# Optimization experiments

Measured on AMD Instinct MI355X. Metric: run time of the kernel, lower is better.

The kernel has to match this reference:

```python
import jax, jax.numpy as jnp
import numpy as np

EPS = 1e-6
NEG_SLOPE = 0.2


def _basis(J):
    # J: [B,N,E,3] -> R: [B,N,E,3(k: U,V,J rows),3(xyz comp)]
    nJ = J / (jnp.linalg.norm(J, axis=-1, keepdims=True) + EPS)
    sub = nJ[..., :2]
    u_z = -(sub[..., 0] ** 2 + sub[..., 1] ** 2) / (nJ[..., 2] + EPS)
    U = jnp.concatenate([sub, u_z[..., None]], axis=-1)
    U = U / (jnp.linalg.norm(U, axis=-1, keepdims=True) + EPS)
    V = jnp.cross(U, nJ)
    return jnp.stack([U, V, nJ], axis=-2)


def _complex_linear(X, J, A, Bw, Cw):
    R = _basis(J)                                   # [B,N,E,3,3], R[...,k,i]
    RtX = jnp.einsum('bneki,bnek->bnei', R, X)      # (R^T X)_i = sum_k R[k,i] X_k
    # rrtx(i, s) has component k equal to R[...,k,i] * s
    a_term = R[..., 0] * RtX[..., 0:1] + R[..., 1] * RtX[..., 1:2]
    b_term = R[..., 1] * RtX[..., 0:1] - R[..., 0] * RtX[..., 1:2]
    c_term = R[..., 2] * RtX[..., 2:3]
    Y = (jnp.einsum('fe,bnei->bnfi', A, a_term)
         + jnp.einsum('fe,bnei->bnfi', Bw, b_term)
         + jnp.einsum('fe,bnei->bnfi', Cw, c_term))
    return Y                                        # [B,N,F,3]


def _vn_leaky_relu(x, W, negative_slope):
    # x: [B,F,3,N]; W: [F,F] torch Linear weight (out,in)
    d = jnp.einsum('gf,bfin->bgin', W, x)
    dot = jnp.sum(x * d, axis=2, keepdims=True)
    d_norm_sq = jnp.sum(d * d, axis=2, keepdims=True)
    neg_branch = x - (dot / (d_norm_sq + EPS)) * d
    lin = jnp.where(dot >= 0, x, neg_branch)
    return negative_slope * x + (1.0 - negative_slope) * lin


def setup_inputs() -> dict:
    key = jax.random.key(0)
    kX, kJ, kA, kB, kC, kW = jax.random.split(key, 6)
    B, N, E, F = 16, 1024, 256, 256
    X = jax.random.normal(kX, (B, N, E, 3), dtype=jnp.float32)
    J = jax.random.normal(kJ, (B, N, E, 3), dtype=jnp.float32)
    A = jax.random.normal(kA, (F, E), dtype=jnp.float32)
    Bw = jax.random.normal(kB, (F, E), dtype=jnp.float32)
    Cw = jax.random.normal(kC, (F, E), dtype=jnp.float32)
    W = jax.random.normal(kW, (F, F), dtype=jnp.float32) * (1.0 / np.sqrt(F))
    return {"X": X, "J": J, "A": A, "Bw": Bw, "Cw": Cw, "W": W, "device": 0}


def reference(X, J, A, Bw, Cw, W, device):
    Y = _complex_linear(X, J, A, Bw, Cw)            # [B,N,F,3]
    x = jnp.transpose(Y, (0, 2, 3, 1))              # [B,F,3,N]
    return _vn_leaky_relu(x, W, NEG_SLOPE)
```

## Files before the change

kernel.cpp:

```cpp
#include <hip/hip_runtime.h>

typedef __attribute__((ext_vector_type(8))) _Float16 half8;
typedef __attribute__((ext_vector_type(4))) _Float16 half4v;
typedef __attribute__((ext_vector_type(4))) float f32x4;
typedef float f32x4u __attribute__((ext_vector_type(4), aligned(4)));
typedef float f32x2u __attribute__((ext_vector_type(2), aligned(4)));

#define EPSF 1e-6f

__device__ __forceinline__ void glds16(const void* g, void* l) {
    __builtin_amdgcn_global_load_lds(
        (const __attribute__((address_space(1))) unsigned*)g,
        (__attribute__((address_space(3))) unsigned*)l, 16, 0, 0);
}
__device__ __forceinline__ unsigned short h2u(_Float16 h) {
    union { _Float16 h; unsigned short u; } c; c.h = h; return c.u;
}

__global__ __launch_bounds__(256) void prep_kernel(
    const float* __restrict__ A, const float* __restrict__ Bw,
    const float* __restrict__ Cw, const float* __restrict__ W,
    _Float16* __restrict__ Mh, _Float16* __restrict__ Wh)
{
    int f = blockIdx.x, e = threadIdx.x;
    Mh[f * 768 + e]       = (_Float16)A[f * 256 + e];
    Mh[f * 768 + 256 + e] = (_Float16)Bw[f * 256 + e];
    Mh[f * 768 + 512 + e] = (_Float16)Cw[f * 256 + e];
    Wh[f * 256 + e]       = (_Float16)W[f * 256 + e];
}

__global__ __launch_bounds__(512, 4) void fused1_kernel(
    const float* __restrict__ X, const float* __restrict__ Jp,
    const _Float16* __restrict__ Mh, _Float16* __restrict__ Y)
{
    __shared__ char lds[55808];
    const int T_OFF = 32768;
    int tid = threadIdx.x;
    int b  = blockIdx.x >> 5;
    int n0 = (blockIdx.x & 31) * 32;

    auto stageA = [&](int buf, int kt) {
        int eb = kt / 3, t = kt % 3;
        int k0 = t * 256 + eb * 32;
        #pragma unroll
        for (int h = 0; h < 2; ++h) {
            int u = h * 512 + tid;
            int row = u >> 2, slot = u & 3;
            size_t go = ((size_t)row * 768 + k0) * 2 + ((slot * 16) ^ ((row & 3) << 4));
            glds16((const char*)Mh + go, lds + buf * 16384 + u * 16);
        }
    };

    int l = tid & 63, lr = l & 15, lq = l >> 4;
    int w = tid >> 6, wc = w & 1, wf = w >> 1;
    int nl = tid >> 4, ep = tid & 15;

    f32x4 acc[3][4] = {};
    stageA(0, 0);

    for (int eb = 0; eb < 8; ++eb) {
        __syncthreads();
        {
            size_t pbase = ((size_t)((b * 1024 + n0 + nl) * 256) + eb * 32 + 2 * ep) * 3;
            f32x4u xa = *(const f32x4u*)(X + pbase);
            f32x2u xb = *(const f32x2u*)(X + pbase + 4);
            f32x4u ja = *(const f32x4u*)(Jp + pbase);
            f32x2u jb = *(const f32x2u*)(Jp + pbase + 4);
            float xs[6] = { xa[0], xa[1], xa[2], xa[3], xb[0], xb[1] };
            float js[6] = { ja[0], ja[1], ja[2], ja[3], jb[0], jb[1] };
            unsigned short hv[2][9];
            #pragma unroll
            for (int p = 0; p < 2; ++p) {
                float x0 = xs[3*p], x1 = xs[3*p+1], x2 = xs[3*p+2];
                float j0 = js[3*p], j1 = js[3*p+1], j2 = js[3*p+2];
                float jj  = j0*j0 + j1*j1 + j2*j2;
                float rn  = __builtin_amdgcn_rcpf(__builtin_amdgcn_sqrtf(jj) + EPSF);
                float nj0 = j0*rn, nj1 = j1*rn, nj2 = j2*rn;
                float s2  = nj0*nj0 + nj1*nj1;
                float uz  = -s2 * __builtin_amdgcn_rcpf(nj2 + EPSF);
                float ru  = __builtin_amdgcn_rcpf(__builtin_amdgcn_sqrtf(s2 + uz*uz) + EPSF);
                float u0 = nj0*ru, u1 = nj1*ru, u2 = uz*ru;
                float v0 = u1*nj2 - u2*nj1;
                float v1 = u2*nj0 - u0*nj2;
                float v2 = u0*nj1 - u1*nj0;
                float r0 = u0*x0 + v0*x1 + nj0*x2;
                float r1 = u1*x0 + v1*x1 + nj1*x2;
                float r2 = u2*x0 + v2*x1 + nj2*x2;
                hv[p][0] = h2u((_Float16)(u0*r0 + u1*r1));
                hv[p][1] = h2u((_Float16)(v0*r0 + v1*r1));
                hv[p][2] = h2u((_Float16)(nj0*r0 + nj1*r1));
                hv[p][3] = h2u((_Float16)(u1*r0 - u0*r1));
                hv[p][4] = h2u((_Float16)(v1*r0 - v0*r1));
                hv[p][5] = h2u((_Float16)(nj1*r0 - nj0*r1));
                hv[p][6] = h2u((_Float16)(u2*r2));
                hv[p][7] = h2u((_Float16)(v2*r2));
                hv[p][8] = h2u((_Float16)(nj2*r2));
            }
            #pragma unroll
            for (int s = 0; s < 9; ++s) {
                int t = s / 3, i = s % 3;
                unsigned pk = (unsigned)hv[0][s] | ((unsigned)hv[1][s] << 16);
                *(unsigned*)(lds + T_OFF + ((t * 96 + i * 32 + nl) * 80) + ep * 4) = pk;
            }
        }
        __syncthreads();
        #pragma unroll
        for (int t = 0; t < 3; ++t) {
            int kt = eb * 3 + t, buf = kt & 1;
            if (kt < 23) stageA(buf ^ 1, kt + 1);
            const char* la = lds + buf * 16384;
            half8 af[4], bf[3];
            #pragma unroll
            for (int mi = 0; mi < 4; ++mi) {
                int f = wf * 64 + mi * 16 + lr;
                af[mi] = *(const half8*)(la + f * 64 + ((lq * 16) ^ ((f & 3) << 4)));
            }
            #pragma unroll
            for (int bi = 0; bi < 3; ++bi) {
                int cr = wc * 48 + bi * 16 + lr;
                bf[bi] = *(const half8*)(lds + T_OFF + (t * 96 + cr) * 80 + lq * 16);
            }
            #pragma unroll
            for (int bi = 0; bi < 3; ++bi)
                #pragma unroll
                for (int mi = 0; mi < 4; ++mi)
                    acc[bi][mi] = __builtin_amdgcn_mfma_f32_16x16x32_f16(af[mi], bf[bi], acc[bi][mi], 0, 0, 0);
            if (t < 2) __syncthreads();
        }
    }

    #pragma unroll
    for (int bi = 0; bi < 3; ++bi) {
        int cr = wc * 48 + bi * 16 + lr;
        int i = cr >> 5, nl2 = cr & 31;
        size_t rowb = ((size_t)b * 3072 + i * 1024 + n0 + nl2) * 256;
        #pragma unroll
        for (int mi = 0; mi < 4; ++mi) {
            int fb = wf * 64 + mi * 16 + lq * 4;
            f32x4 v = acc[bi][mi];
            half4v p;
            p.x = (_Float16)v[0]; p.y = (_Float16)v[1];
            p.z = (_Float16)v[2]; p.w = (_Float16)v[3];
            *(half4v*)(Y + rowb + fb) = p;
        }
    }
}

__global__ __launch_bounds__(256) void gemm2_kernel(
    const _Float16* __restrict__ Wh, const _Float16* __restrict__ Y,
    float* __restrict__ out, int b_off)
{
    __shared__ char lds[65536];
    int tid = threadIdx.x;
    int bid = blockIdx.x;
    int b   = bid / 64;
    int rt  = bid % 64;
    int g0  = (rt >> 4) * 64;
    int n0  = (rt & 15) * 64;
    size_t bC = (size_t)b * 3072;

    auto stage = [&](int buf, int kt) {
        char* la = lds + buf * 32768;
        char* lb = la + 24576;
        int k0 = kt * 64;
        int wv = (tid >> 6) * 1024;
        #pragma unroll
        for (int h = 0; h < 6; ++h) {
            int m = h * 256 + tid;
            int row = m >> 3, slot = m & 7;
            int cg = (row >> 6) * 1024 + n0 + (row & 63);
            unsigned sw = (slot * 16) ^ ((row & 7) << 4);
            size_t go = ((bC + cg) * 256 + k0) * 2 + sw;
            glds16((const char*)Y + go, la + h * 4096 + wv);
        }
        #pragma unroll
        for (int h = 0; h < 2; ++h) {
            int m = h * 256 + tid;
            int row = m >> 3, slot = m & 7;
            unsigned sw = (slot * 16) ^ ((row & 7) << 4);
            size_t go = ((size_t)(g0 + row) * 256 + k0) * 2 + sw;
            glds16((const char*)Wh + go, lb + h * 4096 + wv);
        }
    };

    int l = tid & 63, lr = l & 15, lq = l >> 4;
    int w = tid >> 6, wn = w & 1, wg = w >> 1;

    f32x4 acc[3][2][2] = {};
    stage(0, 0);
    __syncthreads();

    for (int kt = 0; kt < 4; ++kt) {
        int cur = kt & 1;
        if (kt < 3) stage(cur ^ 1, kt + 1);
        const char* la = lds + cur * 32768;
        const char* lb = la + 24576;
        #pragma unroll
        for (int kk = 0; kk < 2; ++kk) {
            half8 af[3][2], bg[2];
            #pragma unroll
            for (int i = 0; i < 3; ++i)
                #pragma unroll
                for (int nc = 0; nc < 2; ++nc) {
                    int R = i * 64 + wn * 32 + nc * 16 + lr;
                    af[i][nc] = *(const half8*)(la + R * 128 + (((kk * 4 + lq) * 16) ^ ((R & 7) << 4)));
                }
            #pragma unroll
            for (int gf = 0; gf < 2; ++gf) {
                int R = wg * 32 + gf * 16 + lr;
                bg[gf] = *(const half8*)(lb + R * 128 + (((kk * 4 + lq) * 16) ^ ((R & 7) << 4)));
            }
            #pragma unroll
            for (int i = 0; i < 3; ++i)
                #pragma unroll
                for (int nc = 0; nc < 2; ++nc)
                    #pragma unroll
                    for (int gf = 0; gf < 2; ++gf)
                        acc[i][nc][gf] = __builtin_amdgcn_mfma_f32_16x16x32_f16(af[i][nc], bg[gf], acc[i][nc][gf], 0, 0, 0);
        }
        __syncthreads();
    }

    int b_g = b_off + b;
    #pragma unroll
    for (int nc = 0; nc < 2; ++nc)
        #pragma unroll
        for (int gf = 0; gf < 2; ++gf) {
            int g  = g0 + wg * 32 + gf * 16 + lr;
            int nb = n0 + wn * 32 + nc * 16 + lq * 4;
            float x[3][4];
            #pragma unroll
            for (int i = 0; i < 3; ++i)
                #pragma unroll
                for (int r = 0; r < 4; ++r)
                    x[i][r] = (float)Y[(bC + i * 1024 + nb + r) * 256 + g];
            f32x4 o[3];
            #pragma unroll
            for (int r = 0; r < 4; ++r) {
                float d0 = acc[0][nc][gf][r], d1 = acc[1][nc][gf][r], d2 = acc[2][nc][gf][r];
                float dot = x[0][r] * d0 + x[1][r] * d1 + x[2][r] * d2;
                float dn  = d0 * d0 + d1 * d1 + d2 * d2;
                float sc  = dot / (dn + EPSF);
                bool pos  = dot >= 0.0f;
                float l0 = pos ? x[0][r] : fmaf(-sc, d0, x[0][r]);
                float l1 = pos ? x[1][r] : fmaf(-sc, d1, x[1][r]);
                float l2 = pos ? x[2][r] : fmaf(-sc, d2, x[2][r]);
                o[0][r] = fmaf(0.8f, l0, 0.2f * x[0][r]);
                o[1][r] = fmaf(0.8f, l1, 0.2f * x[1][r]);
                o[2][r] = fmaf(0.8f, l2, 0.2f * x[2][r]);
            }
            #pragma unroll
            for (int i = 0; i < 3; ++i)
                *(f32x4*)(out + ((size_t)(b_g * 256 + g) * 3 + i) * 1024 + nb) = o[i];
        }
}

extern "C" void kernel_launch(void* const* d_in, const int* in_sizes, int n_in,
                              void* d_out, int out_size, void* d_ws, size_t ws_size,
                              hipStream_t stream)
{
    const float* X  = (const float*)d_in[0];
    const float* J  = (const float*)d_in[1];
    const float* A  = (const float*)d_in[2];
    const float* Bw = (const float*)d_in[3];
    const float* Cw = (const float*)d_in[4];
    const float* W  = (const float*)d_in[5];
    float* out = (float*)d_out;

    char* ws = (char*)d_ws;
    _Float16* Mh = (_Float16*)ws;
    _Float16* Wh = (_Float16*)(ws + 393216);
    _Float16* Y  = (_Float16*)(ws + 524288);

    hipLaunchKernelGGL(prep_kernel,   dim3(256),  dim3(256), 0, stream,
                       A, Bw, Cw, W, Mh, Wh);
    hipLaunchKernelGGL(fused1_kernel, dim3(512),  dim3(512), 0, stream,
                       X, J, Mh, Y);
    hipLaunchKernelGGL(gemm2_kernel,  dim3(1024), dim3(256), 0, stream,
                       Wh, Y, out, 0);
}
```

Before: 67.30 us.

## Double-buffer T tiles in LDS and read weight fragments directly from global

Removes the LDS staging of the weight matrix Mh via global_load_lds and instead loads A fragments straight from global memory (relying on L1/L2 caching). The freed LDS holds two buffers of the transformed X/J tile, so the next e-block's inputs are prefetched into registers and converted after the current MFMAs. This drops from three or four barriers per e-block to one. The cost is uncoalesced, unswizzled global loads for the A operand on every k-step, which may add latency and cache traffic.

After: 91.74 us. +36.3%, slower.

```diff
diff --git a/kernel.cpp b/kernel.cpp
--- a/kernel.cpp
+++ b/kernel.cpp
@@ -33,100 +33,103 @@
     const float* __restrict__ X, const float* __restrict__ Jp,
     const _Float16* __restrict__ Mh, _Float16* __restrict__ Y)
 {
-    __shared__ char lds[55808];
-    const int T_OFF = 32768;
+    __shared__ char lds[46080];
     int tid = threadIdx.x;
     int b  = blockIdx.x >> 5;
     int n0 = (blockIdx.x & 31) * 32;
 
-    auto stageA = [&](int buf, int kt) {
-        int eb = kt / 3, t = kt % 3;
-        int k0 = t * 256 + eb * 32;
-        #pragma unroll
-        for (int h = 0; h < 2; ++h) {
-            int u = h * 512 + tid;
-            int row = u >> 2, slot = u & 3;
-            size_t go = ((size_t)row * 768 + k0) * 2 + ((slot * 16) ^ ((row & 3) << 4));
-            glds16((const char*)Mh + go, lds + buf * 16384 + u * 16);
-        }
-    };
-
     int l = tid & 63, lr = l & 15, lq = l >> 4;
     int w = tid >> 6, wc = w & 1, wf = w >> 1;
     int nl = tid >> 4, ep = tid & 15;
 
+    size_t pb0 = ((size_t)((b * 1024 + n0 + nl) * 256) + 2 * ep) * 3;
+
+    auto computeT = [&](const float* xs, const float* js, char* tb) {
+        unsigned short hv[2][9];
+        #pragma unroll
+        for (int p = 0; p < 2; ++p) {
+            float x0 = xs[3*p], x1 = xs[3*p+1], x2 = xs[3*p+2];
+            float j0 = js[3*p], j1 = js[3*p+1], j2 = js[3*p+2];
+            float jj  = j0*j0 + j1*j1 + j2*j2;
+            float rn  = __builtin_amdgcn_rcpf(__builtin_amdgcn_sqrtf(jj) + EPSF);
+            float nj0 = j0*rn, nj1 = j1*rn, nj2 = j2*rn;
+            float s2  = nj0*nj0 + nj1*nj1;
+            float uz  = -s2 * __builtin_amdgcn_rcpf(nj2 + EPSF);
+            float ru  = __builtin_amdgcn_rcpf(__builtin_amdgcn_sqrtf(s2 + uz*uz) + EPSF);
+            float u0 = nj0*ru, u1 = nj1*ru, u2 = uz*ru;
+            float v0 = u1*nj2 - u2*nj1;
+            float v1 = u2*nj0 - u0*nj2;
+            float v2 = u0*nj1 - u1*nj0;
+            float r0 = u0*x0 + v0*x1 + nj0*x2;
+            float r1 = u1*x0 + v1*x1 + nj1*x2;
+            float r2 = u2*x0 + v2*x1 + nj2*x2;
+            hv[p][0] = h2u((_Float16)(u0*r0 + u1*r1));
+            hv[p][1] = h2u((_Float16)(v0*r0 + v1*r1));
+            hv[p][2] = h2u((_Float16)(nj0*r0 + nj1*r1));
+            hv[p][3] = h2u((_Float16)(u1*r0 - u0*r1));
+            hv[p][4] = h2u((_Float16)(v1*r0 - v0*r1));
+            hv[p][5] = h2u((_Float16)(nj1*r0 - nj0*r1));
+            hv[p][6] = h2u((_Float16)(u2*r2));
+            hv[p][7] = h2u((_Float16)(v2*r2));
+            hv[p][8] = h2u((_Float16)(nj2*r2));
+        }
+        #pragma unroll
+        for (int s = 0; s < 9; ++s) {
+            int t = s / 3, i = s % 3;
+            unsigned pk = (unsigned)hv[0][s] | ((unsigned)hv[1][s] << 16);
+            *(unsigned*)(tb + (t * 96 + i * 32 + nl) * 80 + ep * 4) = pk;
+        }
+    };
+
     f32x4 acc[3][4] = {};
-    stageA(0, 0);
+
+    {
+        f32x4u xa = *(const f32x4u*)(X + pb0);
+        f32x2u xb = *(const f32x2u*)(X + pb0 + 4);
+        f32x4u ja = *(const f32x4u*)(Jp + pb0);
+        f32x2u jb = *(const f32x2u*)(Jp + pb0 + 4);
+        float xs[6] = { xa[0], xa[1], xa[2], xa[3], xb[0], xb[1] };
+        float js[6] = { ja[0], ja[1], ja[2], ja[3], jb[0], jb[1] };
+        computeT(xs, js, lds);
+    }
 
     for (int eb = 0; eb < 8; ++eb) {
+        char* tb  = lds + (eb & 1) * 23040;
+        char* tbn = lds + ((eb & 1) ^ 1) * 23040;
         __syncthreads();
-        {
-            size_t pbase = ((size_t)((b * 1024 + n0 + nl) * 256) + eb * 32 + 2 * ep) * 3;
-            f32x4u xa = *(const f32x4u*)(X + pbase);
-            f32x2u xb = *(const f32x2u*)(X + pbase + 4);
-            f32x4u ja = *(const f32x4u*)(Jp + pbase);
-            f32x2u jb = *(const f32x2u*)(Jp + pbase + 4);
-            float xs[6] = { xa[0], xa[1], xa[2], xa[3], xb[0], xb[1] };
-            float js[6] = { ja[0], ja[1], ja[2], ja[3], jb[0], jb[1] };
-            unsigned short hv[2][9];
-            #pragma unroll
-            for (int p = 0; p < 2; ++p) {
-                float x0 = xs[3*p], x1 = xs[3*p+1], x2 = xs[3*p+2];
-                float j0 = js[3*p], j1 = js[3*p+1], j2 = js[3*p+2];
-                float jj  = j0*j0 + j1*j1 + j2*j2;
-                float rn  = __builtin_amdgcn_rcpf(__builtin_amdgcn_sqrtf(jj) + EPSF);
-                float nj0 = j0*rn, nj1 = j1*rn, nj2 = j2*rn;
-                float s2  = nj0*nj0 + nj1*nj1;
-                float uz  = -s2 * __builtin_amdgcn_rcpf(nj2 + EPSF);
-                float ru  = __builtin_amdgcn_rcpf(__builtin_amdgcn_sqrtf(s2 + uz*uz) + EPSF);
-                float u0 = nj0*ru, u1 = nj1*ru, u2 = uz*ru;
-                float v0 = u1*nj2 - u2*nj1;
-                float v1 = u2*nj0 - u0*nj2;
-                float v2 = u0*nj1 - u1*nj0;
-                float r0 = u0*x0 + v0*x1 + nj0*x2;
-                float r1 = u1*x0 + v1*x1 + nj1*x2;
-                float r2 = u2*x0 + v2*x1 + nj2*x2;
-                hv[p][0] = h2u((_Float16)(u0*r0 + u1*r1));
-                hv[p][1] = h2u((_Float16)(v0*r0 + v1*r1));
-                hv[p][2] = h2u((_Float16)(nj0*r0 + nj1*r1));
-                hv[p][3] = h2u((_Float16)(u1*r0 - u0*r1));
-                hv[p][4] = h2u((_Float16)(v1*r0 - v0*r1));
-                hv[p][5] = h2u((_Float16)(nj1*r0 - nj0*r1));
-                hv[p][6] = h2u((_Float16)(u2*r2));
-                hv[p][7] = h2u((_Float16)(v2*r2));
-                hv[p][8] = h2u((_Float16)(nj2*r2));
-            }
-            #pragma unroll
-            for (int s = 0; s < 9; ++s) {
-                int t = s / 3, i = s % 3;
-                unsigned pk = (unsigned)hv[0][s] | ((unsigned)hv[1][s] << 16);
-                *(unsigned*)(lds + T_OFF + ((t * 96 + i * 32 + nl) * 80) + ep * 4) = pk;
-            }
-        }
-        __syncthreads();
+
+        float xs2[6], js2[6];
+        if (eb < 7) {
+            size_t pb = pb0 + (size_t)(eb + 1) * 96;
+            f32x4u xa = *(const f32x4u*)(X + pb);
+            f32x2u xb = *(const f32x2u*)(X + pb + 4);
+            f32x4u ja = *(const f32x4u*)(Jp + pb);
+            f32x2u jb = *(const f32x2u*)(Jp + pb + 4);
+            xs2[0]=xa[0]; xs2[1]=xa[1]; xs2[2]=xa[2]; xs2[3]=xa[3]; xs2[4]=xb[0]; xs2[5]=xb[1];
+            js2[0]=ja[0]; js2[1]=ja[1]; js2[2]=ja[2]; js2[3]=ja[3]; js2[4]=jb[0]; js2[5]=jb[1];
+        }
+
         #pragma unroll
         for (int t = 0; t < 3; ++t) {
-            int kt = eb * 3 + t, buf = kt & 1;
-            if (kt < 23) stageA(buf ^ 1, kt + 1);
-            const char* la = lds + buf * 16384;
             half8 af[4], bf[3];
             #pragma unroll
             for (int mi = 0; mi < 4; ++mi) {
                 int f = wf * 64 + mi * 16 + lr;
-                af[mi] = *(const half8*)(la + f * 64 + ((lq * 16) ^ ((f & 3) << 4)));
+                af[mi] = *(const half8*)(Mh + (size_t)f * 768 + t * 256 + eb * 32 + lq * 8);
             }
             #pragma unroll
             for (int bi = 0; bi < 3; ++bi) {
                 int cr = wc * 48 + bi * 16 + lr;
-                bf[bi] = *(const half8*)(lds + T_OFF + (t * 96 + cr) * 80 + lq * 16);
+                bf[bi] = *(const half8*)(tb + (t * 96 + cr) * 80 + lq * 16);
             }
             #pragma unroll
             for (int bi = 0; bi < 3; ++bi)
                 #pragma unroll
                 for (int mi = 0; mi < 4; ++mi)
                     acc[bi][mi] = __builtin_amdgcn_mfma_f32_16x16x32_f16(af[mi], bf[bi], acc[bi][mi], 0, 0, 0);
-            if (t < 2) __syncthreads();
-        }
+        }
+
+        if (eb < 7) computeT(xs2, js2, tbn);
     }
 
     #pragma unroll
```
